# Kernel optimization log

Measured on AMD Instinct MI355X. Metric: run time of the kernel, lower is better.

The kernel has to match this reference:

```python
import jax, jax.numpy as jnp
import numpy as np

V, E, H, N, T, L = 32000, 1024, 1024, 64, 32, 196


def setup_inputs() -> dict:
    key = jax.random.key(0)
    ks = jax.random.split(key, 12)
    s = 0.02
    return {
        "inputs": jax.random.randint(ks[0], (N, T), 0, V, dtype=jnp.int32),
        "img_features": jax.random.normal(ks[1], (N, L, H), dtype=jnp.float32),
        "emb": jax.random.normal(ks[2], (V, E), dtype=jnp.float32) * s,
        "w_ih1": jax.random.normal(ks[3], (4 * H, E), dtype=jnp.float32) * s,
        "w_hh1": jax.random.normal(ks[4], (4 * H, H), dtype=jnp.float32) * s,
        "b_ih1": jax.random.normal(ks[5], (4 * H,), dtype=jnp.float32) * s,
        "b_hh1": jax.random.normal(ks[6], (4 * H,), dtype=jnp.float32) * s,
        "w_ih2": jax.random.normal(ks[7], (4 * H, 2 * H), dtype=jnp.float32) * s,
        "w_hh2": jax.random.normal(ks[8], (4 * H, H), dtype=jnp.float32) * s,
        "b_ih2": jax.random.normal(ks[9], (4 * H,), dtype=jnp.float32) * s,
        "b_hh2": jax.random.normal(ks[10], (4 * H,), dtype=jnp.float32) * s,
    }


def _lstm_cell(x, h, c, w_ih, w_hh, b_ih, b_hh):
    # PyTorch LSTMCell: gates ordered i, f, g, o
    g = x @ w_ih.T + b_ih + h @ w_hh.T + b_hh
    i, f, gg, o = jnp.split(g, 4, axis=-1)
    c_new = jax.nn.sigmoid(f) * c + jax.nn.sigmoid(i) * jnp.tanh(gg)
    h_new = jax.nn.sigmoid(o) * jnp.tanh(c_new)
    return h_new, c_new


def reference(inputs, img_features, emb, w_ih1, w_hh1, b_ih1, b_hh1,
              w_ih2, w_hh2, b_ih2, b_hh2):
    n, t = inputs.shape
    hdim = w_hh1.shape[1]
    embedded = emb[inputs]                      # (N, T, E)
    # faithful to original: .view(T, N, -1) is a reshape, NOT a transpose
    xs = embedded.reshape(t, n, -1)             # (T, N, E)

    def step(carry, x_t):
        h1, c1, h2, c2 = carry
        h1, c1 = _lstm_cell(x_t, h1, c1, w_ih1, w_hh1, b_ih1, b_hh1)
        # attention: raw dot-product weights (no softmax in original)
        alpha = jnp.einsum('nd,nld->nl', h1, img_features)   # (N, L)
        v_att = jnp.einsum('nl,nld->nd', alpha, img_features) # (N, D)
        x2 = jnp.concatenate([v_att, h1], axis=1)             # (N, 2H)
        h2, c2 = _lstm_cell(x2, h2, c2, w_ih2, w_hh2, b_ih2, b_hh2)
        return (h1, c1, h2, c2), h2

    zeros = jnp.zeros((n, hdim), dtype=img_features.dtype)
    init = (zeros, zeros, zeros, zeros)
    _, hs = jax.lax.scan(step, init, xs)        # (T, N, H)
    # faithful to original: cat along dim 0 then .view(N, T, -1) == reshape
    return hs.reshape(n, t, -1)
```

## Files before the change

### kernel.cpp

```cpp
#include <hip/hip_runtime.h>
#include <math.h>

typedef __attribute__((ext_vector_type(8))) short bf16x8;
typedef __attribute__((ext_vector_type(4))) short short4v;
typedef __attribute__((ext_vector_type(4))) float f32x4;

__device__ __forceinline__ float sigm(float x) { return 1.f / (1.f + expf(-x)); }

__device__ __forceinline__ float bf2f(short x) {
    unsigned u = ((unsigned)(unsigned short)x) << 16;
    float f; __builtin_memcpy(&f, &u, 4); return f;
}
__device__ __forceinline__ short f2bf(float f) {
    unsigned u; __builtin_memcpy(&u, &f, 4);
    unsigned r = (u + 0x7fffu + ((u >> 16) & 1u)) >> 16;
    return (short)r;
}

__device__ __forceinline__ void grid_barrier(unsigned* slots, unsigned tgt) {
    __syncthreads();
    if (threadIdx.x == 0)
        __hip_atomic_store(slots + (size_t)blockIdx.x * 32, tgt,
                           __ATOMIC_RELAXED, __HIP_MEMORY_SCOPE_AGENT);
    unsigned* my = slots + (size_t)threadIdx.x * 32;
    while (__hip_atomic_load(my, __ATOMIC_RELAXED, __HIP_MEMORY_SCOPE_AGENT) < tgt)
        __builtin_amdgcn_s_sleep(8);
    __syncthreads();
    asm volatile("" ::: "memory");
}

#define OFF_C1      0u
#define OFF_C2      262144u
#define OFF_H2A     524288u
#define OFF_H2B     655360u
#define OFF_H1HI    786432u
#define OFF_H1LO    5111808u
#define OFF_H1F     9437184u
#define OFF_X0HI    17825792u
#define OFF_X0LO    22020096u
#define OFF_B1      26214400u
#define OFF_B2      26230784u
#define OFF_WHH1HI  26247168u
#define OFF_WHH1LO  34635776u
#define OFF_WIH1HI  43024384u
#define OFF_WIH1LO  51412992u
#define OFF_WHH2HI  59801600u
#define OFF_WVHI    68190208u
#define OFF_WVLO    76578816u
#define OFF_WH2HI   84967424u
#define OFF_X12     93356032u

__global__ __launch_bounds__(256) void zero_ws(float4* __restrict__ p) {
    int i = blockIdx.x * 256 + threadIdx.x;
    p[i] = make_float4(0.f, 0.f, 0.f, 0.f);
}

__global__ __launch_bounds__(256) void perm_w_split(const float* __restrict__ src,
                                                    short* __restrict__ hi,
                                                    short* __restrict__ lo,
                                                    int rs, int co) {
    int idx = blockIdx.x * 256 + threadIdx.x;
    int jp = idx >> 8;
    int kq = idx & 255;
    int jsrc = (jp & 3) * 1024 + (jp >> 2);
    float4 v = *(const float4*)(src + (size_t)jsrc * rs + co + kq * 4);
    float a[4] = {v.x, v.y, v.z, v.w};
    short4v h, l;
    #pragma unroll
    for (int e = 0; e < 4; e++) {
        short q = f2bf(a[e]);
        h[e] = q;
        l[e] = f2bf(a[e] - bf2f(q));
    }
    *(short4v*)(hi + (size_t)jp * 1024 + kq * 4) = h;
    *(short4v*)(lo + (size_t)jp * 1024 + kq * 4) = l;
}

__global__ __launch_bounds__(256) void bias_prep(
    const float* __restrict__ bi1, const float* __restrict__ bh1,
    const float* __restrict__ bi2, const float* __restrict__ bh2,
    float* __restrict__ b1p, float* __restrict__ b2p) {
    int jp = blockIdx.x * 256 + threadIdx.x;
    int j = (jp & 3) * 1024 + (jp >> 2);
    b1p[jp] = bi1[j] + bh1[j];
    b2p[jp] = bi2[j] + bh2[j];
}

__global__ __launch_bounds__(256) void gather_x0_split(
    const int* __restrict__ tokens, const float* __restrict__ emb,
    short* __restrict__ hi, short* __restrict__ lo) {
    int idx = blockIdx.x * 256 + threadIdx.x;
    int p = idx >> 8;
    int k0 = (idx & 255) * 4;
    int tok = tokens[p];
    float4 v = *(const float4*)(emb + (size_t)tok * 1024 + k0);
    float a[4] = {v.x, v.y, v.z, v.w};
    short4v h, l;
    #pragma unroll
    for (int e = 0; e < 4; e++) {
        short q = f2bf(a[e]);
        h[e] = q;
        l[e] = f2bf(a[e] - bf2f(q));
    }
    *(short4v*)(hi + (size_t)p * 1024 + k0) = h;
    *(short4v*)(lo + (size_t)p * 1024 + k0) = l;
}

__global__ __launch_bounds__(256) void big_gemm(
    const short* __restrict__ A0, const short* __restrict__ A1s,
    const short* __restrict__ A2s, const short* __restrict__ A3s,
    const short* __restrict__ B0, const short* __restrict__ B1s,
    const short* __restrict__ B2s, const short* __restrict__ B3s,
    const float* __restrict__ bias, float* __restrict__ C, int K) {
    __shared__ short As[128 * 40];
    __shared__ short Bs[128 * 40];
    int tid = threadIdx.x;
    int n0 = blockIdx.x * 128;
    int m0 = blockIdx.y * 128;
    int lane = tid & 63, w = tid >> 6;
    int wm = (w >> 1) * 64, wn = (w & 1) * 64;
    int quad = lane >> 4, l16 = lane & 15;
    int srow = tid >> 2;
    int skc = (tid & 3) * 8;

    f32x4 acc[4][4];
    f32x4 z4 = {0.f, 0.f, 0.f, 0.f};
    #pragma unroll
    for (int i = 0; i < 4; i++)
        #pragma unroll
        for (int j = 0; j < 4; j++) acc[i][j] = z4;

    for (int k0 = 0; k0 < K; k0 += 32) {
        int seg = k0 >> 10;
        const short* Ab = (seg == 0) ? A0 : (seg == 1) ? A1s : (seg == 2) ? A2s : A3s;
        const short* Bb = (seg == 0) ? B0 : (seg == 1) ? B1s : (seg == 2) ? B2s : B3s;
        int kk = (k0 & 1023) + skc;
        const short* ga = Ab + (size_t)(m0 + srow) * 1024 + kk;
        const short* gb = Bb + (size_t)(n0 + srow) * 1024 + kk;
        bf16x8 av0 = *(const bf16x8*)ga;
        bf16x8 av1 = *(const bf16x8*)(ga + 64 * 1024);
        bf16x8 bv0 = *(const bf16x8*)gb;
        bf16x8 bv1 = *(const bf16x8*)(gb + 64 * 1024);
        __syncthreads();
        *(bf16x8*)&As[srow * 40 + skc] = av0;
        *(bf16x8*)&As[(srow + 64) * 40 + skc] = av1;
        *(bf16x8*)&Bs[srow * 40 + skc] = bv0;
        *(bf16x8*)&Bs[(srow + 64) * 40 + skc] = bv1;
        __syncthreads();
        bf16x8 af[4], bfr[4];
        #pragma unroll
        for (int im = 0; im < 4; im++)
            af[im] = *(const bf16x8*)&As[(wm + im * 16 + l16) * 40 + quad * 8];
        #pragma unroll
        for (int in = 0; in < 4; in++)
            bfr[in] = *(const bf16x8*)&Bs[(wn + in * 16 + l16) * 40 + quad * 8];
        #pragma unroll
        for (int im = 0; im < 4; im++)
            #pragma unroll
            for (int in = 0; in < 4; in++)
                acc[im][in] = __builtin_amdgcn_mfma_f32_16x16x32_bf16(
                    af[im], bfr[in], acc[im][in], 0, 0, 0);
    }
    #pragma unroll
    for (int in = 0; in < 4; in++) {
        int j = n0 + wn + in * 16 + l16;
        float bsv = bias[j];
        #pragma unroll
        for (int im = 0; im < 4; im++) {
            #pragma unroll
            for (int r = 0; r < 4; r++) {
                int p = m0 + wm + im * 16 + quad * 4 + r;
                C[(size_t)p * 4096 + j] = acc[im][in][r] + bsv;
            }
        }
    }
}

__global__ __launch_bounds__(256, 1) void lstm1_fused(
    const short* __restrict__ Whi, const short* __restrict__ Wlo,
    const float* __restrict__ X12,
    short* __restrict__ H1hi, short* __restrict__ H1lo,
    float* __restrict__ H1f,
    unsigned* __restrict__ slots) {
    __shared__ short wsh[16 * 1032];
    __shared__ float red[4 * 64 * 16];

    int tid = threadIdx.x;
    int lane = tid & 63, w = tid >> 6;
    int quad = lane >> 4, l16 = lane & 15;
    int g = blockIdx.x;
    int kbase = w * 256;

    for (int i = tid; i < 2048; i += 256) {
        int r = i >> 7;
        int k = (i & 127) * 8;
        *(bf16x8*)&wsh[r * 1032 + k] =
            *(const bf16x8*)(Whi + (size_t)(g * 16 + r) * 1024 + k);
    }

    int s = tid >> 2, dl = tid & 3;
    int d = g * 4 + dl;
    float creg = 0.f;

    __syncthreads();

    const short* bhp = &wsh[l16 * 1032 + kbase + quad * 8];
    const short* blp = Wlo + (size_t)(g * 16 + l16) * 1024 + kbase + quad * 8;

    for (int t = 0; t < 32; t++) {
        f32x4 acc[4];
        f32x4 z4 = {0.f, 0.f, 0.f, 0.f};
        acc[0] = z4; acc[1] = z4; acc[2] = z4; acc[3] = z4;

        if (t > 0) {
            const short* ah = H1hi + (size_t)t * 65536 + (size_t)l16 * 1024 + kbase + quad * 8;
            const short* al = H1lo + (size_t)t * 65536 + (size_t)l16 * 1024 + kbase + quad * 8;
            #pragma unroll
            for (int i = 0; i < 8; i++) {
                int k = i * 32;
                bf16x8 Bh = *(const bf16x8*)(bhp + k);
                bf16x8 Bl = *(const bf16x8*)(blp + k);
                #pragma unroll
                for (int mt = 0; mt < 4; mt++) {
                    bf16x8 Ah = *(const bf16x8*)(ah + mt * 16 * 1024 + k);
                    bf16x8 Al = *(const bf16x8*)(al + mt * 16 * 1024 + k);
                    acc[mt] = __builtin_amdgcn_mfma_f32_16x16x32_bf16(Ah, Bh, acc[mt], 0, 0, 0);
                    acc[mt] = __builtin_amdgcn_mfma_f32_16x16x32_bf16(Al, Bh, acc[mt], 0, 0, 0);
                    acc[mt] = __builtin_amdgcn_mfma_f32_16x16x32_bf16(Ah, Bl, acc[mt], 0, 0, 0);
                }
            }
        }
        #pragma unroll
        for (int mt = 0; mt < 4; mt++)
            #pragma unroll
            for (int r = 0; r < 4; r++) {
                int sr = mt * 16 + quad * 4 + r;
                red[(w * 64 + sr) * 16 + l16] = acc[mt][r];
            }
        __syncthreads();

        float gi = 0.f, gf = 0.f, gg = 0.f, go = 0.f;
        #pragma unroll
        for (int w2 = 0; w2 < 4; w2++) {
            const float* rp = &red[(w2 * 64 + s) * 16 + dl * 4];
            gi += rp[0]; gf += rp[1]; gg += rp[2]; go += rp[3];
        }
        float4 xg = *(const float4*)(X12 + (size_t)t * 262144 + (size_t)s * 4096 + g * 16 + dl * 4);
        gi += xg.x; gf += xg.y; gg += xg.z; go += xg.w;
        float cn = sigm(gf) * creg + sigm(gi) * tanhf(gg);
        creg = cn;
        float hn = sigm(go) * tanhf(cn);
        short q = f2bf(hn);
        short ql = f2bf(hn - bf2f(q));
        __hip_atomic_store(&H1hi[(size_t)(t + 1) * 65536 + s * 1024 + d], q,
                           __ATOMIC_RELAXED, __HIP_MEMORY_SCOPE_AGENT);
        __hip_atomic_store(&H1lo[(size_t)(t + 1) * 65536 + s * 1024 + d], ql,
                           __ATOMIC_RELAXED, __HIP_MEMORY_SCOPE_AGENT);
        H1f[(size_t)t * 65536 + s * 1024 + d] = hn;

        if (t != 31) grid_barrier(slots, (unsigned)(t + 1));
    }
}

__global__ __launch_bounds__(256, 1) void lstm2_fused(
    const short* __restrict__ W, const float* __restrict__ X12,
    short* __restrict__ H2,
    float* __restrict__ out,
    unsigned* __restrict__ slots) {
    __shared__ short wsh[16 * 1032];
    __shared__ float red[4 * 64 * 16];

    int tid = threadIdx.x;
    int lane = tid & 63, w = tid >> 6;
    int quad = lane >> 4, l16 = lane & 15;
    int g = blockIdx.x;
    int kbase = w * 256;

    for (int i = tid; i < 2048; i += 256) {
        int r = i >> 7;
        int k = (i & 127) * 8;
        *(bf16x8*)&wsh[r * 1032 + k] =
            *(const bf16x8*)(W + (size_t)(g * 16 + r) * 1024 + k);
    }

    int s = tid >> 2, dl = tid & 3;
    int d = g * 4 + dl;
    float creg = 0.f;

    __syncthreads();

    const short* bp = &wsh[l16 * 1032 + kbase + quad * 8];

    for (int t = 0; t < 32; t++) {
        f32x4 acc[4];
        f32x4 z4 = {0.f, 0.f, 0.f, 0.f};
        acc[0] = z4; acc[1] = z4; acc[2] = z4; acc[3] = z4;

        if (t > 0) {
            const short* ar = H2 + (size_t)t * 65536 + (size_t)l16 * 1024 + kbase + quad * 8;
            #pragma unroll
            for (int i = 0; i < 8; i++) {
                int k = i * 32;
                bf16x8 b = *(const bf16x8*)(bp + k);
                #pragma unroll
                for (int mt = 0; mt < 4; mt++) {
                    bf16x8 a = *(const bf16x8*)(ar + mt * 16 * 1024 + k);
                    acc[mt] = __builtin_amdgcn_mfma_f32_16x16x32_bf16(a, b, acc[mt], 0, 0, 0);
                }
            }
        }
        #pragma unroll
        for (int mt = 0; mt < 4; mt++)
            #pragma unroll
            for (int r = 0; r < 4; r++) {
                int sr = mt * 16 + quad * 4 + r;
                red[(w * 64 + sr) * 16 + l16] = acc[mt][r];
            }
        __syncthreads();

        float gi = 0.f, gf = 0.f, gg = 0.f, go = 0.f;
        #pragma unroll
        for (int w2 = 0; w2 < 4; w2++) {
            const float* rp = &red[(w2 * 64 + s) * 16 + dl * 4];
            gi += rp[0]; gf += rp[1]; gg += rp[2]; go += rp[3];
        }
        float4 xg = *(const float4*)(X12 + (size_t)t * 262144 + (size_t)s * 4096 + g * 16 + dl * 4);
        gi += xg.x; gf += xg.y; gg += xg.z; go += xg.w;
        float cn = sigm(gf) * creg + sigm(gi) * tanhf(gg);
        creg = cn;
        float hn = sigm(go) * tanhf(cn);
        __hip_atomic_store(&H2[(size_t)(t + 1) * 65536 + s * 1024 + d], f2bf(hn),
                           __ATOMIC_RELAXED, __HIP_MEMORY_SCOPE_AGENT);
        out[(size_t)t * 65536 + s * 1024 + d] = hn;

        if (t != 31) grid_barrier(slots, (unsigned)(t + 1));
    }
}

__global__ __launch_bounds__(256) void attn_batch(
    const float* __restrict__ H1f, const float* __restrict__ F,
    short* __restrict__ Vhi, short* __restrict__ Vlo) {
    __shared__ float vs[4][4][1024];
    int n = blockIdx.x, tg = blockIdx.y;
    int tid = threadIdx.x, lane = tid & 63, w = tid >> 6;

    float h[4][16];
    #pragma unroll
    for (int tt = 0; tt < 4; tt++) {
        const float* hp = H1f + ((size_t)((tg * 4 + tt) * 64 + n)) * 1024 + lane * 16;
        #pragma unroll
        for (int j = 0; j < 4; j++) {
            float4 v = *(const float4*)(hp + j * 4);
            h[tt][j * 4 + 0] = v.x; h[tt][j * 4 + 1] = v.y;
            h[tt][j * 4 + 2] = v.z; h[tt][j * 4 + 3] = v.w;
        }
    }
    float vacc[4][16];
    #pragma unroll
    for (int tt = 0; tt < 4; tt++)
        #pragma unroll
        for (int j = 0; j < 16; j++) vacc[tt][j] = 0.f;

    const float* Fn = F + ((size_t)n * 196) * 1024 + lane * 16;
    for (int l = w; l < 196; l += 4) {
        const float* fr = Fn + (size_t)l * 1024;
        float f[16];
        #pragma unroll
        for (int j = 0; j < 4; j++) {
            float4 v = *(const float4*)(fr + j * 4);
            f[j * 4 + 0] = v.x; f[j * 4 + 1] = v.y;
            f[j * 4 + 2] = v.z; f[j * 4 + 3] = v.w;
        }
        float p[4] = {0.f, 0.f, 0.f, 0.f};
        #pragma unroll
        for (int tt = 0; tt < 4; tt++)
            #pragma unroll
            for (int j = 0; j < 16; j++) p[tt] += f[j] * h[tt][j];
        #pragma unroll
        for (int off = 32; off > 0; off >>= 1) {
            #pragma unroll
            for (int tt = 0; tt < 4; tt++) p[tt] += __shfl_xor(p[tt], off, 64);
        }
        #pragma unroll
        for (int tt = 0; tt < 4; tt++)
            #pragma unroll
            for (int j = 0; j < 16; j++) vacc[tt][j] += p[tt] * f[j];
    }
    #pragma unroll
    for (int tt = 0; tt < 4; tt++)
        #pragma unroll
        for (int j4 = 0; j4 < 4; j4++) {
            float4 v;
            v.x = vacc[tt][j4 * 4 + 0]; v.y = vacc[tt][j4 * 4 + 1];
            v.z = vacc[tt][j4 * 4 + 2]; v.w = vacc[tt][j4 * 4 + 3];
            *(float4*)&vs[w][tt][lane * 16 + j4 * 4] = v;
        }
    __syncthreads();
    int d0 = tid * 4;
    #pragma unroll
    for (int tt = 0; tt < 4; tt++) {
        float4 a = *(const float4*)&vs[0][tt][d0];
        float4 b = *(const float4*)&vs[1][tt][d0];
        float4 cc = *(const float4*)&vs[2][tt][d0];
        float4 e = *(const float4*)&vs[3][tt][d0];
        float sv[4];
        sv[0] = a.x + b.x + cc.x + e.x;
        sv[1] = a.y + b.y + cc.y + e.y;
        sv[2] = a.z + b.z + cc.z + e.z;
        sv[3] = a.w + b.w + cc.w + e.w;
        short4v b1, b2;
        #pragma unroll
        for (int e2 = 0; e2 < 4; e2++) {
            short q = f2bf(sv[e2]);
            b1[e2] = q;
            b2[e2] = f2bf(sv[e2] - bf2f(q));
        }
        size_t row = ((size_t)(tg * 4 + tt) * 64 + n) * 1024 + d0;
        *(short4v*)(Vhi + row) = b1;
        *(short4v*)(Vlo + row) = b2;
    }
}

extern "C" void kernel_launch(void* const* d_in, const int* in_sizes, int n_in,
                              void* d_out, int out_size, void* d_ws, size_t ws_size,
                              hipStream_t stream) {
    const int*   tokens = (const int*)d_in[0];
    const float* imgf   = (const float*)d_in[1];
    const float* emb    = (const float*)d_in[2];
    const float* w_ih1  = (const float*)d_in[3];
    const float* w_hh1  = (const float*)d_in[4];
    const float* b_ih1  = (const float*)d_in[5];
    const float* b_hh1  = (const float*)d_in[6];
    const float* w_ih2  = (const float*)d_in[7];
    const float* w_hh2  = (const float*)d_in[8];
    const float* b_ih2  = (const float*)d_in[9];
    const float* b_hh2  = (const float*)d_in[10];
    float* out = (float*)d_out;
    char* ws = (char*)d_ws;

    unsigned* slots1 = (unsigned*)(ws + OFF_C1);
    unsigned* slots2 = (unsigned*)(ws + OFF_C1 + 32768u);
    short* H1hi   = (short*)(ws + OFF_H1HI);
    short* H1lo   = (short*)(ws + OFF_H1LO);
    float* H1f    = (float*)(ws + OFF_H1F);
    short* H2     = (short*)(ws + OFF_H1F);
    short* X0hi   = (short*)(ws + OFF_X0HI);
    short* X0lo   = (short*)(ws + OFF_X0LO);
    short* Vhi    = (short*)(ws + OFF_X0HI);
    short* Vlo    = (short*)(ws + OFF_X0LO);
    float* bias1p = (float*)(ws + OFF_B1);
    float* bias2p = (float*)(ws + OFF_B2);
    short* whh1hi = (short*)(ws + OFF_WHH1HI);
    short* whh1lo = (short*)(ws + OFF_WHH1LO);
    short* wih1hi = (short*)(ws + OFF_WIH1HI);
    short* wih1lo = (short*)(ws + OFF_WIH1LO);
    short* whh2hi = (short*)(ws + OFF_WHH2HI);
    short* wvhi   = (short*)(ws + OFF_WVHI);
    short* wvlo   = (short*)(ws + OFF_WVLO);
    short* wh2hi  = (short*)(ws + OFF_WH2HI);
    float* X12    = (float*)(ws + OFF_X12);
    short* dump   = (short*)(ws + OFF_X12);

    zero_ws<<<16, 256, 0, stream>>>((float4*)(ws + OFF_C1));
    perm_w_split<<<4096, 256, 0, stream>>>(w_hh1, whh1hi, whh1lo, 1024, 0);
    perm_w_split<<<4096, 256, 0, stream>>>(w_ih1, wih1hi, wih1lo, 1024, 0);
    perm_w_split<<<4096, 256, 0, stream>>>(w_hh2, whh2hi, dump, 1024, 0);
    perm_w_split<<<4096, 256, 0, stream>>>(w_ih2, wvhi, wvlo, 2048, 0);
    perm_w_split<<<4096, 256, 0, stream>>>(w_ih2, wh2hi, dump, 2048, 1024);
    bias_prep<<<16, 256, 0, stream>>>(b_ih1, b_hh1, b_ih2, b_hh2, bias1p, bias2p);
    gather_x0_split<<<2048, 256, 0, stream>>>(tokens, emb, X0hi, X0lo);

    big_gemm<<<dim3(32, 16), 256, 0, stream>>>(
        X0hi, X0lo, X0hi, X0hi,
        wih1hi, wih1hi, wih1lo, wih1hi,
        bias1p, X12, 3072);

    lstm1_fused<<<256, 256, 0, stream>>>(
        whh1hi, whh1lo, X12, H1hi, H1lo, H1f, slots1);

    attn_batch<<<dim3(64, 8), 256, 0, stream>>>(H1f, imgf, Vhi, Vlo);

    big_gemm<<<dim3(32, 16), 256, 0, stream>>>(
        Vhi, Vlo, Vhi, H1hi + 65536,
        wvhi, wvhi, wvlo, wh2hi,
        bias2p, X12, 4096);

    lstm2_fused<<<256, 256, 0, stream>>>(
        whh2hi, X12, H2, out, slots2);
}
```

Measured before the change: 1.113 ms.

## Replace all-to-all grid barrier with master-release barrier and prefetch next-step inputs

Replaces the grid barrier, in which every block polled all 256 arrival slots, with a centralized one: block 0 polls the arrival slots and then writes a single release flag that the other blocks spin on. It also moves the fp32 hidden-state/output store and the load of the next step's input-gate row into the window between arriving and waiting, so that memory latency overlaps the barrier. Flags use system-scope atomics and a shorter sleep. The cost is an extra hop through block 0 before other blocks are released, and possible extra traffic from system-scope polling.

```diff
diff --git a/kernel.cpp b/kernel.cpp
--- a/kernel.cpp
+++ b/kernel.cpp
@@ -17,22 +17,15 @@
     return (short)r;
 }
 
-__device__ __forceinline__ void grid_barrier(unsigned* slots, unsigned tgt) {
-    __syncthreads();
-    if (threadIdx.x == 0)
-        __hip_atomic_store(slots + (size_t)blockIdx.x * 32, tgt,
-                           __ATOMIC_RELAXED, __HIP_MEMORY_SCOPE_AGENT);
-    unsigned* my = slots + (size_t)threadIdx.x * 32;
-    while (__hip_atomic_load(my, __ATOMIC_RELAXED, __HIP_MEMORY_SCOPE_AGENT) < tgt)
-        __builtin_amdgcn_s_sleep(8);
-    __syncthreads();
-    asm volatile("" ::: "memory");
+__device__ __forceinline__ unsigned sys_ld(const unsigned* p) {
+    return __hip_atomic_load(p, __ATOMIC_RELAXED, __HIP_MEMORY_SCOPE_SYSTEM);
+}
+__device__ __forceinline__ void sys_st(unsigned* p, unsigned v) {
+    __hip_atomic_store(p, v, __ATOMIC_RELAXED, __HIP_MEMORY_SCOPE_SYSTEM);
 }
 
 #define OFF_C1      0u
 #define OFF_C2      262144u
-#define OFF_H2A     524288u
-#define OFF_H2B     655360u
 #define OFF_H1HI    786432u
 #define OFF_H1LO    5111808u
 #define OFF_H1F     9437184u
@@ -53,6 +46,11 @@
 __global__ __launch_bounds__(256) void zero_ws(float4* __restrict__ p) {
     int i = blockIdx.x * 256 + threadIdx.x;
     p[i] = make_float4(0.f, 0.f, 0.f, 0.f);
+}
+
+__global__ __launch_bounds__(256) void zero_slots(unsigned* __restrict__ p) {
+    int i = blockIdx.x * 256 + threadIdx.x;
+    __hip_atomic_store(p + i, 0u, __ATOMIC_RELAXED, __HIP_MEMORY_SCOPE_SYSTEM);
 }
 
 __global__ __launch_bounds__(256) void perm_w_split(const float* __restrict__ src,
@@ -181,7 +179,7 @@
     const float* __restrict__ X12,
     short* __restrict__ H1hi, short* __restrict__ H1lo,
     float* __restrict__ H1f,
-    unsigned* __restrict__ slots) {
+    unsigned* __restrict__ arrive, unsigned* __restrict__ release) {
     __shared__ short wsh[16 * 1032];
     __shared__ float red[4 * 64 * 16];
 
@@ -206,6 +204,9 @@
 
     const short* bhp = &wsh[l16 * 1032 + kbase + quad * 8];
     const short* blp = Wlo + (size_t)(g * 16 + l16) * 1024 + kbase + quad * 8;
+    const float* xgp = X12 + (size_t)s * 4096 + g * 16 + dl * 4;
+
+    float4 xg = *(const float4*)xgp;
 
     for (int t = 0; t < 32; t++) {
         f32x4 acc[4];
@@ -245,7 +246,6 @@
             const float* rp = &red[(w2 * 64 + s) * 16 + dl * 4];
             gi += rp[0]; gf += rp[1]; gg += rp[2]; go += rp[3];
         }
-        float4 xg = *(const float4*)(X12 + (size_t)t * 262144 + (size_t)s * 4096 + g * 16 + dl * 4);
         gi += xg.x; gf += xg.y; gg += xg.z; go += xg.w;
         float cn = sigm(gf) * creg + sigm(gi) * tanhf(gg);
         creg = cn;
@@ -256,9 +256,26 @@
                            __ATOMIC_RELAXED, __HIP_MEMORY_SCOPE_AGENT);
         __hip_atomic_store(&H1lo[(size_t)(t + 1) * 65536 + s * 1024 + d], ql,
                            __ATOMIC_RELAXED, __HIP_MEMORY_SCOPE_AGENT);
-        H1f[(size_t)t * 65536 + s * 1024 + d] = hn;
-
-        if (t != 31) grid_barrier(slots, (unsigned)(t + 1));
+        __syncthreads();
+        if (t != 31) {
+            unsigned tgt = (unsigned)(t + 1);
+            if (tid == 0) sys_st(arrive + (size_t)g * 32, tgt);
+            H1f[(size_t)t * 65536 + s * 1024 + d] = hn;
+            xg = *(const float4*)(xgp + (size_t)(t + 1) * 262144);
+            if (g == 0) {
+                unsigned* my = arrive + (size_t)tid * 32;
+                while (sys_ld(my) < tgt) __builtin_amdgcn_s_sleep(2);
+                __syncthreads();
+                if (tid == 0) sys_st(release, tgt);
+            } else {
+                if (tid == 0)
+                    while (sys_ld(release) < tgt) __builtin_amdgcn_s_sleep(2);
+                __syncthreads();
+            }
+            asm volatile("" ::: "memory");
+        } else {
+            H1f[(size_t)t * 65536 + s * 1024 + d] = hn;
+        }
     }
 }
 
@@ -266,7 +283,7 @@
     const short* __restrict__ W, const float* __restrict__ X12,
     short* __restrict__ H2,
     float* __restrict__ out,
-    unsigned* __restrict__ slots) {
+    unsigned* __restrict__ arrive, unsigned* __restrict__ release) {
     __shared__ short wsh[16 * 1032];
     __shared__ float red[4 * 64 * 16];
 
@@ -290,6 +307,9 @@
     __syncthreads();
 
     const short* bp = &wsh[l16 * 1032 + kbase + quad * 8];
+    const float* xgp = X12 + (size_t)s * 4096 + g * 16 + dl * 4;
+
+    float4 xg = *(const float4*)xgp;
 
     for (int t = 0; t < 32; t++) {
         f32x4 acc[4];
@@ -324,16 +344,32 @@
             const float* rp = &red[(w2 * 64 + s) * 16 + dl * 4];
             gi += rp[0]; gf += rp[1]; gg += rp[2]; go += rp[3];
         }
-        float4 xg = *(const float4*)(X12 + (size_t)t * 262144 + (size_t)s * 4096 + g * 16 + dl * 4);
         gi += xg.x; gf += xg.y; gg += xg.z; go += xg.w;
         float cn = sigm(gf) * creg + sigm(gi) * tanhf(gg);
         creg = cn;
         float hn = sigm(go) * tanhf(cn);
         __hip_atomic_store(&H2[(size_t)(t + 1) * 65536 + s * 1024 + d], f2bf(hn),
                            __ATOMIC_RELAXED, __HIP_MEMORY_SCOPE_AGENT);
-        out[(size_t)t * 65536 + s * 1024 + d] = hn;
-
-        if (t != 31) grid_barrier(slots, (unsigned)(t + 1));
+        __syncthreads();
+        if (t != 31) {
+            unsigned tgt = (unsigned)(t + 1);
+            if (tid == 0) sys_st(arrive + (size_t)g * 32, tgt);
+            out[(size_t)t * 65536 + s * 1024 + d] = hn;
+            xg = *(const float4*)(xgp + (size_t)(t + 1) * 262144);
+            if (g == 0) {
+                unsigned* my = arrive + (size_t)tid * 32;
+                while (sys_ld(my) < tgt) __builtin_amdgcn_s_sleep(2);
+                __syncthreads();
+                if (tid == 0) sys_st(release, tgt);
+            } else {
+                if (tid == 0)
+                    while (sys_ld(release) < tgt) __builtin_amdgcn_s_sleep(2);
+                __syncthreads();
+            }
+            asm volatile("" ::: "memory");
+        } else {
+            out[(size_t)t * 65536 + s * 1024 + d] = hn;
+        }
     }
 }
 
@@ -438,8 +474,10 @@
     float* out = (float*)d_out;
     char* ws = (char*)d_ws;
 
-    unsigned* slots1 = (unsigned*)(ws + OFF_C1);
-    unsigned* slots2 = (unsigned*)(ws + OFF_C1 + 32768u);
+    unsigned* arrive1  = (unsigned*)(ws + OFF_C1);
+    unsigned* release1 = (unsigned*)(ws + OFF_C1 + 32768u);
+    unsigned* arrive2  = (unsigned*)(ws + OFF_C1 + 65536u);
+    unsigned* release2 = (unsigned*)(ws + OFF_C1 + 98304u);
     short* H1hi   = (short*)(ws + OFF_H1HI);
     short* H1lo   = (short*)(ws + OFF_H1LO);
     float* H1f    = (float*)(ws + OFF_H1F);
@@ -461,7 +499,7 @@
     float* X12    = (float*)(ws + OFF_X12);
     short* dump   = (short*)(ws + OFF_X12);
 
-    zero_ws<<<16, 256, 0, stream>>>((float4*)(ws + OFF_C1));
+    zero_slots<<<128, 256, 0, stream>>>((unsigned*)(ws + OFF_C1));
     perm_w_split<<<4096, 256, 0, stream>>>(w_hh1, whh1hi, whh1lo, 1024, 0);
     perm_w_split<<<4096, 256, 0, stream>>>(w_ih1, wih1hi, wih1lo, 1024, 0);
     perm_w_split<<<4096, 256, 0, stream>>>(w_hh2, whh2hi, dump, 1024, 0);
@@ -476,7 +514,7 @@
         bias1p, X12, 3072);
 
     lstm1_fused<<<256, 256, 0, stream>>>(
-        whh1hi, whh1lo, X12, H1hi, H1lo, H1f, slots1);
+        whh1hi, whh1lo, X12, H1hi, H1lo, H1f, arrive1, release1);
 
     attn_batch<<<dim3(64, 8), 256, 0, stream>>>(H1f, imgf, Vhi, Vlo);
 
@@ -486,5 +524,5 @@
         bias2p, X12, 4096);
 
     lstm2_fused<<<256, 256, 0, stream>>>(
-        whh2hi, X12, H2, out, slots2);
-}
+        whh2hi, X12, H2, out, arrive2, release2);
+}
```

Measured after the change: 1.043 ms. 6.3% less time.
